# Optimization experiments

Hardware: AMD Instinct MI355X
Metric: run time of the kernel (lower is better)

## Reference

```python
import jax, jax.numpy as jnp
import numpy as np
import math

D_MODEL = 1024
NUM_HEADS = 16
HEAD_DIM = D_MODEL // NUM_HEADS
BATCH = 2
SEQ = 2048
THETA = 10000.0


def _rope_tables(seq_len, head_dim, theta=THETA):
    inv_freq = 1.0 / theta ** (jnp.arange(0, head_dim, 2, dtype=jnp.float32) / head_dim)
    pos = jnp.arange(seq_len, dtype=jnp.float32)
    freqs = jnp.outer(pos, inv_freq)                 # [S, hd/2]
    emb = jnp.concatenate([freqs, freqs], axis=-1)   # [S, hd]
    return jnp.cos(emb), jnp.sin(emb)


def _rotate_half(x):
    x1, x2 = jnp.split(x, 2, axis=-1)
    return jnp.concatenate([-x2, x1], axis=-1)


def setup_inputs() -> dict:
    key = jax.random.key(0)
    k1, k2, k3 = jax.random.split(key, 3)
    x = jax.random.normal(k1, (BATCH, SEQ, D_MODEL), dtype=jnp.float32)
    # causal mask: 1 where attend allowed, 0 where masked
    mask = jnp.tril(jnp.ones((SEQ, SEQ), dtype=jnp.int32))[None, None]
    w_qkv = jax.random.normal(k2, (D_MODEL, 3 * D_MODEL), dtype=jnp.float32) / math.sqrt(D_MODEL)
    w_out = jax.random.normal(k3, (D_MODEL, D_MODEL), dtype=jnp.float32) / math.sqrt(D_MODEL)
    return {"x": x, "mask": mask, "w_qkv": w_qkv, "w_out": w_out}


def reference(x, mask, w_qkv, w_out):
    B, S, _ = x.shape
    qkv = x @ w_qkv                                          # [B,S,3*D]
    qkv = qkv.reshape(B, S, 3, NUM_HEADS, HEAD_DIM)
    qkv = jnp.transpose(qkv, (2, 0, 3, 1, 4))                # [3,B,H,S,hd]
    q, k, v = qkv[0], qkv[1], qkv[2]
    cos, sin = _rope_tables(S, HEAD_DIM)                     # [S,hd]
    cos = cos[None, None]; sin = sin[None, None]
    q = q * cos + _rotate_half(q) * sin
    k = k * cos + _rotate_half(k) * sin
    scores = jnp.einsum('bhqd,bhkd->bhqk', q, k) / math.sqrt(HEAD_DIM)
    scores = jnp.where(mask == 0, -jnp.inf, scores)
    attn = jax.nn.softmax(scores, axis=-1)                   # dropout p=0 (eval)
    out = jnp.einsum('bhqk,bhkd->bhqd', attn, v)             # [B,H,S,hd]
    out = jnp.transpose(out, (0, 2, 1, 3)).reshape(B, S, D_MODEL)
    return out @ w_out
```

## Files before the change

kernel.cpp:

```cpp
#include <hip/hip_runtime.h>

typedef __bf16 bf16;
typedef __bf16 bf16x4 __attribute__((ext_vector_type(4)));
typedef __bf16 bf16x8 __attribute__((ext_vector_type(8)));
typedef short s16x4 __attribute__((ext_vector_type(4)));
typedef float f32x4 __attribute__((ext_vector_type(4)));

constexpr int BATCH = 2;
constexpr int SEQ   = 2048;
constexpr int DMODEL= 1024;
constexpr int NH    = 16;
constexpr int HD    = 64;
constexpr int M_ROWS= BATCH * SEQ;
constexpr int N_QKV = 3 * DMODEL;

__device__ __forceinline__ void gl_lds16(const bf16* g, bf16* l) {
  __builtin_amdgcn_global_load_lds(
      (const __attribute__((address_space(1))) unsigned int*)g,
      (__attribute__((address_space(3))) unsigned int*)l, 16, 0, 0);
}

__device__ __forceinline__ f32x4 mfma_16x16x16_bf16(bf16x4 a, bf16x4 b,
                                                    f32x4 c) {
#if defined(__HIP_DEVICE_COMPILE__)
  union { bf16x4 h; s16x4 s; } ua{a}, ub{b};
  return __builtin_amdgcn_mfma_f32_16x16x16bf16_1k(ua.s, ub.s, c, 0, 0, 0);
#else
  return c;
#endif
}

__global__ __launch_bounds__(256) void transpose_cast_kernel(
    const float* __restrict__ src, bf16* __restrict__ dst, int R, int C) {
  __shared__ float tile[32][33];
  const int c0 = blockIdx.x * 32, r0 = blockIdx.y * 32;
  const int tx = threadIdx.x, ty = threadIdx.y;
#pragma unroll
  for (int i = 0; i < 4; i++)
    tile[ty + 8 * i][tx] = src[(size_t)(r0 + ty + 8 * i) * C + c0 + tx];
  __syncthreads();
#pragma unroll
  for (int i = 0; i < 4; i++)
    dst[(size_t)(c0 + ty + 8 * i) * R + r0 + tx] = (bf16)tile[tx][ty + 8 * i];
}

__global__ __launch_bounds__(256) void cast_f32_bf16(
    const float* __restrict__ src, bf16* __restrict__ dst) {
  const int i = (blockIdx.x * 256 + threadIdx.x) * 8;
  float4 f0 = *(const float4*)&src[i];
  float4 f1 = *(const float4*)&src[i + 4];
  bf16x8 v;
  v[0] = (bf16)f0.x; v[1] = (bf16)f0.y; v[2] = (bf16)f0.z; v[3] = (bf16)f0.w;
  v[4] = (bf16)f1.x; v[5] = (bf16)f1.y; v[6] = (bf16)f1.z; v[7] = (bf16)f1.w;
  *(bf16x8*)&dst[i] = v;
}

#define GEMM_BODY(A, BT, K)                                                    \
  __shared__ bf16 As[128 * 32];                                                \
  __shared__ bf16 Bs[128 * 32];                                                \
  const int t = threadIdx.x;                                                   \
  const int m0 = blockIdx.y * 128;                                             \
  const int n0 = blockIdx.x * 128;                                             \
  const int w = t >> 6, lane = t & 63, g = lane >> 4, li = lane & 15;          \
  const int r0w = (w & 1) * 64, c0w = (w >> 1) * 64;                           \
  f32x4 acc[4][4] = {};                                                        \
  for (int k0 = 0; k0 < (K); k0 += 32) {                                       \
    __syncthreads();                                                           \
    _Pragma("unroll") for (int c = 0; c < 2; c++) {                            \
      const int idx = (w * 2 + c) * 64 + lane;                                 \
      const int row = idx >> 2, col = (idx & 3) * 8;                           \
      gl_lds16(&(A)[(size_t)(m0 + row) * (K) + k0 + col],                      \
               &As[(w * 2 + c) * 512]);                                        \
      gl_lds16(&(BT)[(size_t)(n0 + row) * (K) + k0 + col],                     \
               &Bs[(w * 2 + c) * 512]);                                        \
    }                                                                          \
    __syncthreads();                                                           \
    bf16x8 a[4], b[4];                                                         \
    _Pragma("unroll") for (int mt = 0; mt < 4; mt++)                           \
        a[mt] = *(const bf16x8*)&As[(r0w + mt * 16 + li) * 32 + g * 8];        \
    _Pragma("unroll") for (int nt = 0; nt < 4; nt++)                           \
        b[nt] = *(const bf16x8*)&Bs[(c0w + nt * 16 + li) * 32 + g * 8];        \
    _Pragma("unroll") for (int mt = 0; mt < 4; mt++)                           \
        _Pragma("unroll") for (int nt = 0; nt < 4; nt++)                       \
            acc[mt][nt] = __builtin_amdgcn_mfma_f32_16x16x32_bf16(             \
                a[mt], b[nt], acc[mt][nt], 0, 0, 0);                           \
  }

__global__ __launch_bounds__(256) void gemm_out64(
    const bf16* __restrict__ A, const bf16* __restrict__ BT,
    float* __restrict__ C, int M, int N, int K) {
  __shared__ bf16 As[64 * 32];
  __shared__ bf16 Bs[128 * 32];
  const int t = threadIdx.x;
  const int m0 = blockIdx.y * 64;
  const int n0 = blockIdx.x * 128;
  const int w = t >> 6, lane = t & 63, g = lane >> 4, li = lane & 15;
  const int r0w = (w & 1) * 32, c0w = (w >> 1) * 64;
  f32x4 acc[2][4] = {};
  for (int k0 = 0; k0 < K; k0 += 32) {
    __syncthreads();
    {
      const int idx = w * 64 + lane;
      const int row = idx >> 2, col = (idx & 3) * 8;
      gl_lds16(&A[(size_t)(m0 + row) * K + k0 + col], &As[w * 512]);
    }
#pragma unroll
    for (int c = 0; c < 2; c++) {
      const int idx = (w * 2 + c) * 64 + lane;
      const int row = idx >> 2, col = (idx & 3) * 8;
      gl_lds16(&BT[(size_t)(n0 + row) * K + k0 + col], &Bs[(w * 2 + c) * 512]);
    }
    __syncthreads();
    bf16x8 a[2], b[4];
#pragma unroll
    for (int mt = 0; mt < 2; mt++)
      a[mt] = *(const bf16x8*)&As[(r0w + mt * 16 + li) * 32 + g * 8];
#pragma unroll
    for (int nt = 0; nt < 4; nt++)
      b[nt] = *(const bf16x8*)&Bs[(c0w + nt * 16 + li) * 32 + g * 8];
#pragma unroll
    for (int mt = 0; mt < 2; mt++)
#pragma unroll
      for (int nt = 0; nt < 4; nt++)
        acc[mt][nt] = __builtin_amdgcn_mfma_f32_16x16x32_bf16(
            a[mt], b[nt], acc[mt][nt], 0, 0, 0);
  }
#pragma unroll
  for (int mt = 0; mt < 2; mt++)
#pragma unroll
    for (int nt = 0; nt < 4; nt++)
#pragma unroll
      for (int r = 0; r < 4; r++) {
        const int m = m0 + r0w + mt * 16 + g * 4 + r;
        const int n = n0 + c0w + nt * 16 + li;
        C[(size_t)m * N + n] = acc[mt][nt][r];
      }
}

__global__ __launch_bounds__(256) void gemm_qkv_rope(
    const bf16* __restrict__ A, const bf16* __restrict__ BT,
    bf16* __restrict__ Qb, bf16* __restrict__ Kb, bf16* __restrict__ Vt) {
  constexpr int K = DMODEL;
  GEMM_BODY(A, BT, K)

  const int region = n0 >> 10;
  const int b = m0 >> 11;
  const int h = ((n0 + c0w) >> 6) & 15;
  const size_t bh = (size_t)(b * NH + h);

  if (region < 2) {
    bf16* dst = region == 0 ? Qb : Kb;
    const float outsc = region == 0 ? 0.125f * 1.44269504f : 1.f;
    const float L = 13.287712379549449f;
    const float if0 = exp2f(-(float)(2 * li) / 64.f * L);
    const float if1 = exp2f(-(float)(2 * (li + 16)) / 64.f * L);
#pragma unroll
    for (int mt = 0; mt < 4; mt++)
#pragma unroll
      for (int r = 0; r < 4; r++) {
        const int s = (m0 + r0w + mt * 16 + g * 4 + r) & (SEQ - 1);
        float cs[2], sn[2];
        __sincosf((float)s * if0, &sn[0], &cs[0]);
        __sincosf((float)s * if1, &sn[1], &cs[1]);
#pragma unroll
        for (int nt = 0; nt < 4; nt++) {
          const int d = nt * 16 + li;
          const int par = nt & 1;
          const float a = acc[mt][nt][r];
          const float ap = acc[mt][nt ^ 2][r];
          const float v = (nt < 2) ? a * cs[par] - ap * sn[par]
                                   : a * cs[par] + ap * sn[par];
          dst[(bh * SEQ + s) * HD + d] = (bf16)(v * outsc);
        }
      }
  } else {
#pragma unroll
    for (int mt = 0; mt < 4; mt++)
#pragma unroll
      for (int nt = 0; nt < 4; nt++) {
        const int s = (m0 + r0w + mt * 16 + g * 4) & (SEQ - 1);
        const int d = nt * 16 + li;
        bf16x4 v;
#pragma unroll
        for (int r = 0; r < 4; r++) v[r] = (bf16)acc[mt][nt][r];
        *(bf16x4*)&Vt[(bh * HD + d) * SEQ + s] = v;
      }
  }
}

__global__ __launch_bounds__(256, 2) void flash_attn10(
    const bf16* __restrict__ Q, const bf16* __restrict__ Kb,
    const bf16* __restrict__ Vt, bf16* __restrict__ Oout) {
  const int bx = blockIdx.x;
  const int bh = bx & 31;
  const int pr = bx >> 5;
  const int t = threadIdx.x, w = t >> 6, lane = t & 63, g = lane >> 4,
            li = lane & 15;

  __shared__ bf16 Ks[2][4096];
  __shared__ bf16 Vs[2][4096];

  const bf16* Qh = Q  + (size_t)bh * SEQ * HD;
  const bf16* Kh = Kb + (size_t)bh * SEQ * HD;
  const bf16* Vh = Vt + (size_t)bh * HD * SEQ;
  const int b = bh >> 4, h = bh & 15;

  bf16x4 ones;
#pragma unroll
  for (int r = 0; r < 4; r++) ones[r] = (bf16)1.f;

  const int p0 = w * 128 + lane, p1 = p0 + 64;
  const int sr0 = p0 >> 3, sc0 = ((p0 & 7) ^ (sr0 & 7)) * 8;
  const int sr1 = p1 >> 3, sc1 = ((p1 & 7) ^ (sr1 & 7)) * 8;
  const int lo0 = w * 1024, lo1 = w * 1024 + 512;

  for (int seg = 0; seg < 2; seg++) {
    const int qt = seg ? 31 - pr : pr;
    const int q0 = qt * 64;
    const int qw = q0 + w * 16;
    const int jend = q0 + 64;

    bf16x8 qf[2];
#pragma unroll
    for (int ks = 0; ks < 2; ks++)
      qf[ks] = *(const bf16x8*)&Qh[(size_t)(qw + li) * HD + ks * 32 + g * 8];

    f32x4 o[4] = {};
    f32x4 o4  = {};

    gl_lds16(&Kh[(size_t)sr0 * HD + sc0], &Ks[0][lo0]);
    gl_lds16(&Kh[(size_t)sr1 * HD + sc1], &Ks[0][lo1]);
    gl_lds16(&Vh[(size_t)sr0 * SEQ + sc0], &Vs[0][lo0]);
    gl_lds16(&Vh[(size_t)sr1 * SEQ + sc1], &Vs[0][lo1]);
    __syncthreads();

    for (int j0 = 0; j0 < jend; j0 += 64) {
      const int cur = (j0 >> 6) & 1, nxt = cur ^ 1;
      if (j0 + 64 < jend) {
        const int jn = j0 + 64;
        gl_lds16(&Kh[(size_t)(jn + sr0) * HD + sc0], &Ks[nxt][lo0]);
        gl_lds16(&Kh[(size_t)(jn + sr1) * HD + sc1], &Ks[nxt][lo1]);
        gl_lds16(&Vh[(size_t)sr0 * SEQ + jn + sc0], &Vs[nxt][lo0]);
        gl_lds16(&Vh[(size_t)sr1 * SEQ + jn + sc1], &Vs[nxt][lo1]);
      }

      if (j0 <= qw + 15) {
        const bool masked = (j0 + 63 > qw);
        const int ntlim = min(4, ((qw + 15 - j0) >> 4) + 1);

        f32x4 sacc[4] = {};
#pragma unroll
        for (int ks = 0; ks < 2; ks++)
#pragma unroll
          for (int nt = 0; nt < 4; nt++) {
            if (nt >= ntlim) continue;
            const int rK = nt * 16 + li;
            const int pK = rK * 8 + ((ks * 4 + g) ^ (li & 7));
            bf16x8 kf = *(const bf16x8*)&Ks[cur][pK * 8];
            sacc[nt] = __builtin_amdgcn_mfma_f32_16x16x32_bf16(
                kf, qf[ks], sacc[nt], 0, 0, 0);
          }

        bf16x4 pf[4];
#pragma unroll
        for (int nt = 0; nt < 4; nt++) {
          if (nt >= ntlim) continue;
#pragma unroll
          for (int r = 0; r < 4; r++) {
            float v = sacc[nt][r];
            if (masked) {
              const int kk = j0 + nt * 16 + g * 4 + r;
              v = (kk <= qw + li) ? v : -1e30f;
            }
            pf[nt][r] = (bf16)exp2f(v);
          }
        }

#pragma unroll
        for (int nt = 0; nt < 4; nt++) {
          if (nt >= ntlim) continue;
          o4 = mfma_16x16x16_bf16(ones, pf[nt], o4);
#pragma unroll
          for (int dt = 0; dt < 4; dt++) {
            const int rV = dt * 16 + li;
            const int cg = nt * 2 + (g >> 1);
            const int pV = rV * 8 + (cg ^ (rV & 7));
            bf16x4 vfrag = *(const bf16x4*)&Vs[cur][pV * 8 + (g & 1) * 4];
            o[dt] = mfma_16x16x16_bf16(vfrag, pf[nt], o[dt]);
          }
        }
      }
      __syncthreads();
    }

    const float inv_l = 1.f / o4[0];
    const int s = qw + li;
#pragma unroll
    for (int dt = 0; dt < 4; dt++) {
      bf16x4 ov;
#pragma unroll
      for (int r = 0; r < 4; r++) ov[r] = (bf16)(o[dt][r] * inv_l);
      *(bf16x4*)&Oout[((size_t)(b * SEQ + s)) * DMODEL + h * 64 + dt * 16 +
                      g * 4] = ov;
    }
  }
}

extern "C" void kernel_launch(void* const* d_in, const int* in_sizes, int n_in,
                              void* d_out, int out_size, void* d_ws,
                              size_t ws_size, hipStream_t stream) {
  const float* x     = (const float*)d_in[0];
  const float* w_qkv = (const float*)d_in[2];
  const float* w_out = (const float*)d_in[3];
  float* out = (float*)d_out;

  char* ws = (char*)d_ws;
  bf16* WqkvT = (bf16*)(ws);
  bf16* WoutT = (bf16*)(ws + 6291456);
  bf16* xb    = (bf16*)(ws + 8388608);
  bf16* Qb    = (bf16*)(ws + 16777216);
  bf16* Kbuf  = (bf16*)(ws + 25165824);
  bf16* Vt    = (bf16*)(ws + 33554432);
  bf16* attn  = (bf16*)(ws + 41943040);

  cast_f32_bf16<<<M_ROWS * DMODEL / 2048, 256, 0, stream>>>(x, xb);
  transpose_cast_kernel<<<dim3(N_QKV / 32, DMODEL / 32), dim3(32, 8), 0,
                          stream>>>(w_qkv, WqkvT, DMODEL, N_QKV);
  transpose_cast_kernel<<<dim3(DMODEL / 32, DMODEL / 32), dim3(32, 8), 0,
                          stream>>>(w_out, WoutT, DMODEL, DMODEL);
  gemm_qkv_rope<<<dim3(N_QKV / 128, M_ROWS / 128), 256, 0, stream>>>(
      xb, WqkvT, Qb, Kbuf, Vt);
  flash_attn10<<<dim3(512), 256, 0, stream>>>(Qb, Kbuf, Vt, attn);
  gemm_out64<<<dim3(DMODEL / 128, M_ROWS / 64), 256, 0, stream>>>(
      attn, WoutT, out, M_ROWS, DMODEL, DMODEL);
}
```

Before: 221.5 us.

## Fuse prep kernels, stage RoPE output through LDS, split attention into per-tile blocks

Merges the x cast and both weight transpose-casts into one prep kernel, removing two launches. The QKV GEMM epilogue now writes rotated Q/K into a padded shared-memory tile, then stores full 16-byte rows to global memory instead of scattered 2-byte stores. The attention kernel drops its paired-tile loop (one block per two query tiles) and launches one block per query tile, with heaviest tiles first and a higher occupancy hint. Load balance now depends on scheduling order rather than pairing, and the larger shared buffer in the GEMM may reduce occupancy.

```diff
diff --git a/kernel.cpp b/kernel.cpp
--- a/kernel.cpp
+++ b/kernel.cpp
@@ -30,11 +30,35 @@
 #endif
 }
 
-__global__ __launch_bounds__(256) void transpose_cast_kernel(
-    const float* __restrict__ src, bf16* __restrict__ dst, int R, int C) {
+__global__ __launch_bounds__(256) void prep_kernel(
+    const float* __restrict__ x, const float* __restrict__ w_qkv,
+    const float* __restrict__ w_out, bf16* __restrict__ xb,
+    bf16* __restrict__ WqkvT, bf16* __restrict__ WoutT) {
+  const int bx = blockIdx.x, t = threadIdx.x;
+  if (bx < 2048) {
+    const int i = (bx * 256 + t) * 8;
+    float4 f0 = *(const float4*)&x[i];
+    float4 f1 = *(const float4*)&x[i + 4];
+    bf16x8 v;
+    v[0] = (bf16)f0.x; v[1] = (bf16)f0.y; v[2] = (bf16)f0.z; v[3] = (bf16)f0.w;
+    v[4] = (bf16)f1.x; v[5] = (bf16)f1.y; v[6] = (bf16)f1.z; v[7] = (bf16)f1.w;
+    *(bf16x8*)&xb[i] = v;
+    return;
+  }
   __shared__ float tile[32][33];
-  const int c0 = blockIdx.x * 32, r0 = blockIdx.y * 32;
-  const int tx = threadIdx.x, ty = threadIdx.y;
+  const float* src;
+  bf16* dst;
+  int R, C, c0, r0;
+  if (bx < 5120) {
+    const int idx = bx - 2048;
+    src = w_qkv; dst = WqkvT; R = DMODEL; C = N_QKV;
+    c0 = (idx % 96) * 32; r0 = (idx / 96) * 32;
+  } else {
+    const int idx = bx - 5120;
+    src = w_out; dst = WoutT; R = DMODEL; C = DMODEL;
+    c0 = (idx & 31) * 32; r0 = (idx >> 5) * 32;
+  }
+  const int tx = t & 31, ty = t >> 5;
 #pragma unroll
   for (int i = 0; i < 4; i++)
     tile[ty + 8 * i][tx] = src[(size_t)(r0 + ty + 8 * i) * C + c0 + tx];
@@ -44,20 +68,10 @@
     dst[(size_t)(c0 + ty + 8 * i) * R + r0 + tx] = (bf16)tile[tx][ty + 8 * i];
 }
 
-__global__ __launch_bounds__(256) void cast_f32_bf16(
-    const float* __restrict__ src, bf16* __restrict__ dst) {
-  const int i = (blockIdx.x * 256 + threadIdx.x) * 8;
-  float4 f0 = *(const float4*)&src[i];
-  float4 f1 = *(const float4*)&src[i + 4];
-  bf16x8 v;
-  v[0] = (bf16)f0.x; v[1] = (bf16)f0.y; v[2] = (bf16)f0.z; v[3] = (bf16)f0.w;
-  v[4] = (bf16)f1.x; v[5] = (bf16)f1.y; v[6] = (bf16)f1.z; v[7] = (bf16)f1.w;
-  *(bf16x8*)&dst[i] = v;
-}
-
 #define GEMM_BODY(A, BT, K)                                                    \
-  __shared__ bf16 As[128 * 32];                                                \
-  __shared__ bf16 Bs[128 * 32];                                                \
+  __shared__ bf16 smem[8448];                                                  \
+  bf16* As = smem;                                                             \
+  bf16* Bs = smem + 4096;                                                      \
   const int t = threadIdx.x;                                                   \
   const int m0 = blockIdx.y * 128;                                             \
   const int n0 = blockIdx.x * 128;                                             \
@@ -154,25 +168,40 @@
     const float L = 13.287712379549449f;
     const float if0 = exp2f(-(float)(2 * li) / 64.f * L);
     const float if1 = exp2f(-(float)(2 * (li + 16)) / 64.f * L);
-#pragma unroll
-    for (int mt = 0; mt < 4; mt++)
-#pragma unroll
-      for (int r = 0; r < 4; r++) {
-        const int s = (m0 + r0w + mt * 16 + g * 4 + r) & (SEQ - 1);
-        float cs[2], sn[2];
-        __sincosf((float)s * if0, &sn[0], &cs[0]);
-        __sincosf((float)s * if1, &sn[1], &cs[1]);
-#pragma unroll
-        for (int nt = 0; nt < 4; nt++) {
-          const int d = nt * 16 + li;
-          const int par = nt & 1;
-          const float a = acc[mt][nt][r];
-          const float ap = acc[mt][nt ^ 2][r];
-          const float v = (nt < 2) ? a * cs[par] - ap * sn[par]
-                                   : a * cs[par] + ap * sn[par];
-          dst[(bh * SEQ + s) * HD + d] = (bf16)(v * outsc);
+    bf16* lw = smem + w * 2112;
+#pragma unroll
+    for (int pass = 0; pass < 2; pass++) {
+      __syncthreads();
+#pragma unroll
+      for (int mtl = 0; mtl < 2; mtl++) {
+        const int mt = pass * 2 + mtl;
+#pragma unroll
+        for (int r = 0; r < 4; r++) {
+          const int s = (m0 + r0w + mt * 16 + g * 4 + r) & (SEQ - 1);
+          float cs[2], sn[2];
+          __sincosf((float)s * if0, &sn[0], &cs[0]);
+          __sincosf((float)s * if1, &sn[1], &cs[1]);
+#pragma unroll
+          for (int nt = 0; nt < 4; nt++) {
+            const int par = nt & 1;
+            const float a = acc[mt][nt][r];
+            const float ap = acc[mt][nt ^ 2][r];
+            const float v = (nt < 2) ? a * cs[par] - ap * sn[par]
+                                     : a * cs[par] + ap * sn[par];
+            lw[(mtl * 16 + g * 4 + r) * 66 + nt * 16 + li] =
+                (bf16)(v * outsc);
+          }
         }
       }
+      __syncthreads();
+      const int rowl = lane >> 1, dh = (lane & 1) * 32;
+      const int s = (m0 + r0w + pass * 32 + rowl) & (SEQ - 1);
+      bf16* gdst = &dst[(bh * SEQ + s) * HD + dh];
+      const bf16* lsrc = &lw[rowl * 66 + dh];
+#pragma unroll
+      for (int c = 0; c < 4; c++)
+        *(bf16x8*)&gdst[c * 8] = *(const bf16x8*)&lsrc[c * 8];
+    }
   } else {
 #pragma unroll
     for (int mt = 0; mt < 4; mt++)
@@ -188,12 +217,13 @@
   }
 }
 
-__global__ __launch_bounds__(256, 2) void flash_attn10(
+__global__ __launch_bounds__(256, 4) void flash_attn8(
     const bf16* __restrict__ Q, const bf16* __restrict__ Kb,
     const bf16* __restrict__ Vt, bf16* __restrict__ Oout) {
   const int bx = blockIdx.x;
+  const int qt = 31 - (bx >> 5);
   const int bh = bx & 31;
-  const int pr = bx >> 5;
+  const int q0 = qt * 64;
   const int t = threadIdx.x, w = t >> 6, lane = t & 63, g = lane >> 4,
             li = lane & 15;
 
@@ -203,8 +233,16 @@
   const bf16* Qh = Q  + (size_t)bh * SEQ * HD;
   const bf16* Kh = Kb + (size_t)bh * SEQ * HD;
   const bf16* Vh = Vt + (size_t)bh * HD * SEQ;
-  const int b = bh >> 4, h = bh & 15;
-
+
+  const int qw = q0 + w * 16;
+
+  bf16x8 qf[2];
+#pragma unroll
+  for (int ks = 0; ks < 2; ks++)
+    qf[ks] = *(const bf16x8*)&Qh[(size_t)(qw + li) * HD + ks * 32 + g * 8];
+
+  f32x4 o[4] = {};
+  f32x4 o4  = {};
   bf16x4 ones;
 #pragma unroll
   for (int r = 0; r < 4; r++) ones[r] = (bf16)1.f;
@@ -214,95 +252,84 @@
   const int sr1 = p1 >> 3, sc1 = ((p1 & 7) ^ (sr1 & 7)) * 8;
   const int lo0 = w * 1024, lo1 = w * 1024 + 512;
 
-  for (int seg = 0; seg < 2; seg++) {
-    const int qt = seg ? 31 - pr : pr;
-    const int q0 = qt * 64;
-    const int qw = q0 + w * 16;
-    const int jend = q0 + 64;
-
-    bf16x8 qf[2];
-#pragma unroll
-    for (int ks = 0; ks < 2; ks++)
-      qf[ks] = *(const bf16x8*)&Qh[(size_t)(qw + li) * HD + ks * 32 + g * 8];
-
-    f32x4 o[4] = {};
-    f32x4 o4  = {};
-
-    gl_lds16(&Kh[(size_t)sr0 * HD + sc0], &Ks[0][lo0]);
-    gl_lds16(&Kh[(size_t)sr1 * HD + sc1], &Ks[0][lo1]);
-    gl_lds16(&Vh[(size_t)sr0 * SEQ + sc0], &Vs[0][lo0]);
-    gl_lds16(&Vh[(size_t)sr1 * SEQ + sc1], &Vs[0][lo1]);
-    __syncthreads();
-
-    for (int j0 = 0; j0 < jend; j0 += 64) {
-      const int cur = (j0 >> 6) & 1, nxt = cur ^ 1;
-      if (j0 + 64 < jend) {
-        const int jn = j0 + 64;
-        gl_lds16(&Kh[(size_t)(jn + sr0) * HD + sc0], &Ks[nxt][lo0]);
-        gl_lds16(&Kh[(size_t)(jn + sr1) * HD + sc1], &Ks[nxt][lo1]);
-        gl_lds16(&Vh[(size_t)sr0 * SEQ + jn + sc0], &Vs[nxt][lo0]);
-        gl_lds16(&Vh[(size_t)sr1 * SEQ + jn + sc1], &Vs[nxt][lo1]);
-      }
-
-      if (j0 <= qw + 15) {
-        const bool masked = (j0 + 63 > qw);
-        const int ntlim = min(4, ((qw + 15 - j0) >> 4) + 1);
-
-        f32x4 sacc[4] = {};
-#pragma unroll
-        for (int ks = 0; ks < 2; ks++)
-#pragma unroll
-          for (int nt = 0; nt < 4; nt++) {
-            if (nt >= ntlim) continue;
-            const int rK = nt * 16 + li;
-            const int pK = rK * 8 + ((ks * 4 + g) ^ (li & 7));
-            bf16x8 kf = *(const bf16x8*)&Ks[cur][pK * 8];
-            sacc[nt] = __builtin_amdgcn_mfma_f32_16x16x32_bf16(
-                kf, qf[ks], sacc[nt], 0, 0, 0);
-          }
-
-        bf16x4 pf[4];
+  const int jend = q0 + 64;
+
+  gl_lds16(&Kh[(size_t)sr0 * HD + sc0], &Ks[0][lo0]);
+  gl_lds16(&Kh[(size_t)sr1 * HD + sc1], &Ks[0][lo1]);
+  gl_lds16(&Vh[(size_t)sr0 * SEQ + sc0], &Vs[0][lo0]);
+  gl_lds16(&Vh[(size_t)sr1 * SEQ + sc1], &Vs[0][lo1]);
+  __syncthreads();
+
+  for (int j0 = 0; j0 < jend; j0 += 64) {
+    const int cur = (j0 >> 6) & 1, nxt = cur ^ 1;
+    if (j0 + 64 < jend) {
+      const int jn = j0 + 64;
+      gl_lds16(&Kh[(size_t)(jn + sr0) * HD + sc0], &Ks[nxt][lo0]);
+      gl_lds16(&Kh[(size_t)(jn + sr1) * HD + sc1], &Ks[nxt][lo1]);
+      gl_lds16(&Vh[(size_t)sr0 * SEQ + jn + sc0], &Vs[nxt][lo0]);
+      gl_lds16(&Vh[(size_t)sr1 * SEQ + jn + sc1], &Vs[nxt][lo1]);
+    }
+
+    if (j0 <= qw + 15) {
+      const bool masked = (j0 + 63 > qw);
+      const int ntlim = min(4, ((qw + 15 - j0) >> 4) + 1);
+
+      f32x4 sacc[4] = {};
+#pragma unroll
+      for (int ks = 0; ks < 2; ks++)
 #pragma unroll
         for (int nt = 0; nt < 4; nt++) {
           if (nt >= ntlim) continue;
-#pragma unroll
-          for (int r = 0; r < 4; r++) {
-            float v = sacc[nt][r];
-            if (masked) {
-              const int kk = j0 + nt * 16 + g * 4 + r;
-              v = (kk <= qw + li) ? v : -1e30f;
-            }
-            pf[nt][r] = (bf16)exp2f(v);
+          const int rK = nt * 16 + li;
+          const int pK = rK * 8 + ((ks * 4 + g) ^ (li & 7));
+          bf16x8 kf = *(const bf16x8*)&Ks[cur][pK * 8];
+          sacc[nt] = __builtin_amdgcn_mfma_f32_16x16x32_bf16(kf, qf[ks],
+                                                             sacc[nt], 0, 0, 0);
+        }
+
+      bf16x4 pf[4];
+#pragma unroll
+      for (int nt = 0; nt < 4; nt++) {
+        if (nt >= ntlim) continue;
+#pragma unroll
+        for (int r = 0; r < 4; r++) {
+          float v = sacc[nt][r];
+          if (masked) {
+            const int kk = j0 + nt * 16 + g * 4 + r;
+            v = (kk <= qw + li) ? v : -1e30f;
           }
+          pf[nt][r] = (bf16)exp2f(v);
         }
-
-#pragma unroll
-        for (int nt = 0; nt < 4; nt++) {
-          if (nt >= ntlim) continue;
-          o4 = mfma_16x16x16_bf16(ones, pf[nt], o4);
-#pragma unroll
-          for (int dt = 0; dt < 4; dt++) {
-            const int rV = dt * 16 + li;
-            const int cg = nt * 2 + (g >> 1);
-            const int pV = rV * 8 + (cg ^ (rV & 7));
-            bf16x4 vfrag = *(const bf16x4*)&Vs[cur][pV * 8 + (g & 1) * 4];
-            o[dt] = mfma_16x16x16_bf16(vfrag, pf[nt], o[dt]);
-          }
+      }
+
+#pragma unroll
+      for (int nt = 0; nt < 4; nt++) {
+        if (nt >= ntlim) continue;
+        o4 = mfma_16x16x16_bf16(ones, pf[nt], o4);
+#pragma unroll
+        for (int dt = 0; dt < 4; dt++) {
+          const int rV = dt * 16 + li;
+          const int cg = nt * 2 + (g >> 1);
+          const int pV = rV * 8 + (cg ^ (rV & 7));
+          bf16x4 vfrag = *(const bf16x4*)&Vs[cur][pV * 8 + (g & 1) * 4];
+          o[dt] = mfma_16x16x16_bf16(vfrag, pf[nt], o[dt]);
         }
       }
-      __syncthreads();
-    }
-
-    const float inv_l = 1.f / o4[0];
-    const int s = qw + li;
-#pragma unroll
-    for (int dt = 0; dt < 4; dt++) {
-      bf16x4 ov;
-#pragma unroll
-      for (int r = 0; r < 4; r++) ov[r] = (bf16)(o[dt][r] * inv_l);
-      *(bf16x4*)&Oout[((size_t)(b * SEQ + s)) * DMODEL + h * 64 + dt * 16 +
-                      g * 4] = ov;
-    }
+    }
+    __syncthreads();
+  }
+
+  const float inv_l = 1.f / o4[0];
+
+  const int b = bh >> 4, h = bh & 15;
+  const int s = qw + li;
+#pragma unroll
+  for (int dt = 0; dt < 4; dt++) {
+    bf16x4 ov;
+#pragma unroll
+    for (int r = 0; r < 4; r++) ov[r] = (bf16)(o[dt][r] * inv_l);
+    *(bf16x4*)&Oout[((size_t)(b * SEQ + s)) * DMODEL + h * 64 + dt * 16 +
+                    g * 4] = ov;
   }
 }
 
@@ -323,14 +350,11 @@
   bf16* Vt    = (bf16*)(ws + 33554432);
   bf16* attn  = (bf16*)(ws + 41943040);
 
-  cast_f32_bf16<<<M_ROWS * DMODEL / 2048, 256, 0, stream>>>(x, xb);
-  transpose_cast_kernel<<<dim3(N_QKV / 32, DMODEL / 32), dim3(32, 8), 0,
-                          stream>>>(w_qkv, WqkvT, DMODEL, N_QKV);
-  transpose_cast_kernel<<<dim3(DMODEL / 32, DMODEL / 32), dim3(32, 8), 0,
-                          stream>>>(w_out, WoutT, DMODEL, DMODEL);
+  prep_kernel<<<dim3(6144), 256, 0, stream>>>(x, w_qkv, w_out, xb, WqkvT,
+                                              WoutT);
   gemm_qkv_rope<<<dim3(N_QKV / 128, M_ROWS / 128), 256, 0, stream>>>(
       xb, WqkvT, Qb, Kbuf, Vt);
-  flash_attn10<<<dim3(512), 256, 0, stream>>>(Qb, Kbuf, Vt, attn);
+  flash_attn8<<<dim3(1024), 256, 0, stream>>>(Qb, Kbuf, Vt, attn);
   gemm_out64<<<dim3(DMODEL / 128, M_ROWS / 64), 256, 0, stream>>>(
       attn, WoutT, out, M_ROWS, DMODEL, DMODEL);
 }
```

Result: faster. 208.9 us (-5.7%).
